# Optimization experiments

Measured on AMD Instinct MI355X. Metric: run time of the kernel, lower is better.

Reference implementation:

```python
import math
import jax, jax.numpy as jnp
import numpy as np

N_HEADS = 16

def setup_inputs() -> dict:
    key = jax.random.key(0)
    k1, k2, k3 = jax.random.split(key, 3)
    B, T, C = 4, 2048, 1024
    alpha = 0.5
    std = alpha * (1.0 / C) ** 0.5
    x = jax.random.normal(k1, (B, T, C), dtype=jnp.float32)
    w_attn = jax.random.normal(k2, (C, 3 * C), dtype=jnp.float32) * std
    b_attn = jnp.zeros((3 * C,), dtype=jnp.float32)
    w_proj = jax.random.normal(k3, (C, C), dtype=jnp.float32) * std
    b_proj = jnp.zeros((C,), dtype=jnp.float32)
    return {"x": x, "w_attn": w_attn, "b_attn": b_attn, "w_proj": w_proj, "b_proj": b_proj}

def reference(x, w_attn, b_attn, w_proj, b_proj):
    B, T, C = x.shape
    H = N_HEADS
    D = C // H
    qkv = x @ w_attn + b_attn                      # [B,T,3C]
    q, k, v = jnp.split(qkv, 3, axis=-1)
    # [B,T,C] -> [B,H,T,D]
    q = q.reshape(B, T, H, D).transpose(0, 2, 1, 3)
    k = k.reshape(B, T, H, D).transpose(0, 2, 1, 3)
    v = v.reshape(B, T, H, D).transpose(0, 2, 1, 3)
    att = jnp.einsum('bhqd,bhkd->bhqk', q, k) * (1.0 / math.sqrt(D))
    causal = jnp.tril(jnp.ones((T, T), dtype=bool))
    att = jnp.where(causal, att, -jnp.inf)
    att = jax.nn.softmax(att, axis=-1)
    y = jnp.einsum('bhqk,bhkd->bhqd', att, v)      # [B,H,T,D]
    y = y.transpose(0, 2, 1, 3).reshape(B, T, C)
    return y @ w_proj + b_proj
```

## Files before the change

kernel.cpp:

```cpp
#include <hip/hip_runtime.h>
#include <hip/hip_bf16.h>

typedef __bf16 bf16x8 __attribute__((ext_vector_type(8)));
typedef float f32x4 __attribute__((ext_vector_type(4)));
typedef unsigned short u16x8 __attribute__((ext_vector_type(8)));
typedef unsigned short u16x4 __attribute__((ext_vector_type(4)));

#define HB 16
#define TT 2048
#define CCH 1024
#define DD 64

#define AS1 __attribute__((address_space(1)))
#define AS3 __attribute__((address_space(3)))
#define GL16(gp, lp) __builtin_amdgcn_global_load_lds((const AS1 void*)(gp), (AS3 void*)(lp), 16, 0, 0)

__device__ __forceinline__ unsigned short f2bf(float f) {
  union { __hip_bfloat16 h; unsigned short u; } cv;
  cv.h = __float2bfloat16(f);
  return cv.u;
}

__device__ __forceinline__ f32x4 mfma16(bf16x8 a, bf16x8 b, f32x4 c) {
  return __builtin_amdgcn_mfma_f32_16x16x32_bf16(a, b, c, 0, 0, 0);
}


__global__ __launch_bounds__(256) void cvt_f32_bf16(const float* __restrict__ in,
                                                    unsigned short* __restrict__ out,
                                                    int n4) {
  int i = blockIdx.x * 256 + threadIdx.x;
  if (i >= n4) return;
  float4 v = reinterpret_cast<const float4*>(in)[i];
  u16x4 o;
  o.x = f2bf(v.x); o.y = f2bf(v.y); o.z = f2bf(v.z); o.w = f2bf(v.w);
  *reinterpret_cast<u16x4*>(out + (size_t)i * 4) = o;
}

__global__ __launch_bounds__(256) void transpose_cvt(const float* __restrict__ w,
                                                     unsigned short* __restrict__ wt,
                                                     int N) {
  __shared__ unsigned short t[32][33];
  int nb = blockIdx.x * 32, kb = blockIdx.y * 32;
  int tx = threadIdx.x & 31, ty = threadIdx.x >> 5;
  #pragma unroll
  for (int r = 0; r < 32; r += 8)
    t[ty + r][tx] = f2bf(w[(size_t)(kb + ty + r) * N + nb + tx]);
  __syncthreads();
  #pragma unroll
  for (int r = 0; r < 32; r += 8)
    wt[(size_t)(nb + ty + r) * 1024 + kb + tx] = t[tx][ty + r];
}


template <int EPI>
__global__ __launch_bounds__(256) void gemm_bf16(
    const unsigned short* __restrict__ A,
    const unsigned short* __restrict__ Bt,
    const float* __restrict__ bias,
    float* __restrict__ outf,
    unsigned short* __restrict__ qb,
    unsigned short* __restrict__ kb,
    unsigned short* __restrict__ vt,
    int nbx, int wpx) {
  __shared__ unsigned short As[8192];
  __shared__ unsigned short Bs[8192];
  const int bid = blockIdx.x;
  const int work = (bid & 7) * wpx + (bid >> 3);
  const int m0 = (work / nbx) * 128, n0 = (work % nbx) * 128;
  const int tid = threadIdx.x;
  const int lane = tid & 63;
  const int wid = tid >> 6;
  const int r16 = lane & 15, g = lane >> 4;
  const int wm = wid >> 1, wn = wid & 1;
  const int srow = tid >> 3;
  const int schx = (tid & 7) ^ (srow & 7);

  f32x4 acc[4][4];
  #pragma unroll
  for (int i = 0; i < 4; ++i)
    #pragma unroll
    for (int j = 0; j < 4; ++j) acc[i][j] = (f32x4){0.f, 0.f, 0.f, 0.f};

  const int rx = r16 & 7;

  for (int kt = 0; kt < 1024; kt += 64) {
    #pragma unroll
    for (int i = 0; i < 4; ++i) {
      const int row = i * 32 + srow;
      GL16(A + (size_t)(m0 + row) * 1024 + kt + schx * 8, As + i * 2048 + tid * 8);
    }
    #pragma unroll
    for (int i = 0; i < 4; ++i) {
      const int row = i * 32 + srow;
      GL16(Bt + (size_t)(n0 + row) * 1024 + kt + schx * 8, Bs + i * 2048 + tid * 8);
    }
    __syncthreads();
    #pragma unroll
    for (int h = 0; h < 2; ++h) {
      bf16x8 af[4], bfr[4];
      #pragma unroll
      for (int i = 0; i < 4; ++i)
        af[i] = *reinterpret_cast<const bf16x8*>(
            &As[(wm * 64 + i * 16 + r16) * 64 + ((g + 4 * h) ^ rx) * 8]);
      #pragma unroll
      for (int j = 0; j < 4; ++j)
        bfr[j] = *reinterpret_cast<const bf16x8*>(
            &Bs[(wn * 64 + j * 16 + r16) * 64 + ((g + 4 * h) ^ rx) * 8]);
      #pragma unroll
      for (int i = 0; i < 4; ++i)
        #pragma unroll
        for (int j = 0; j < 4; ++j)
          acc[i][j] = mfma16(af[i], bfr[j], acc[i][j]);
    }
    __syncthreads();
  }

  #pragma unroll
  for (int i = 0; i < 4; ++i) {
    #pragma unroll
    for (int j = 0; j < 4; ++j) {
      const int n = n0 + wn * 64 + j * 16 + r16;
      const int mbase = m0 + wm * 64 + i * 16 + g * 4;
      const float bi = bias[n];
      if (EPI == 1) {
        #pragma unroll
        for (int r = 0; r < 4; ++r)
          outf[(size_t)(mbase + r) * 1024 + n] = acc[i][j][r] + bi;
      } else {
        const int which = n >> 10;
        const int cc2 = n & 1023;
        const int h = cc2 >> 6, d = cc2 & 63;
        const int b = mbase >> 11, t = mbase & 2047;
        if (which == 2) {
          u16x4 o;
          #pragma unroll
          for (int r = 0; r < 4; ++r) o[r] = f2bf(acc[i][j][r] + bi);
          *reinterpret_cast<u16x4*>(
              &vt[(((size_t)b * HB + h) * DD + d) * TT + t]) = o;
        } else {
          unsigned short* dst = (which == 0) ? qb : kb;
          const float sc = (which == 0) ? 0.18033688011112042f : 1.0f;
          #pragma unroll
          for (int r = 0; r < 4; ++r)
            dst[(((size_t)b * HB + h) * TT + (t + r)) * DD + d] =
                f2bf((acc[i][j][r] + bi) * sc);
        }
      }
    }
  }
}


__global__ __launch_bounds__(512, 2) void attn_kernel(
    const unsigned short* __restrict__ qg_,
    const unsigned short* __restrict__ kg_,
    const unsigned short* __restrict__ vtg_,
    unsigned short* __restrict__ yb) {
  const int bid = blockIdx.x;
  const int work = (bid & 7) * 64 + (bid >> 3);
  const int bh = work >> 3;
  const int jb = work & 7;
  const int tid = threadIdx.x;
  const int wid = tid >> 6;
  const int lane = tid & 63;
  const int r16 = lane & 15, g = lane >> 4;
  const unsigned short* Q = qg_ + (size_t)bh * TT * DD;
  const unsigned short* K = kg_ + (size_t)bh * TT * DD;
  const unsigned short* Vt = vtg_ + (size_t)bh * DD * TT;
  const int b = bh >> 4, h = bh & 15;

  __shared__ unsigned short smem[2][16384];

  const int krow0 = tid >> 3;
  const int kchx = (tid & 7) ^ (krow0 & 7);
  const int vd0 = tid >> 4;
  const int vchx = (tid & 15) ^ (vd0 & 7);
  const int rx = r16 & 7;

#define STAGE(bi, kvb_) do {                                                      \
    unsigned short* sb_ = &smem[bi][0];                                           \
    const unsigned short* gk_ = K + (size_t)(kvb_) * DD;                          \
    GL16(gk_ + (size_t)krow0 * DD + kchx * 8,              sb_ + tid * 8);        \
    GL16(gk_ + (size_t)(64 + krow0) * DD + kchx * 8,       sb_ + 4096 + tid * 8); \
    GL16(Vt + (size_t)vd0 * TT + (kvb_) + vchx * 8,        sb_ + 8192 + tid * 8); \
    GL16(Vt + (size_t)(32 + vd0) * TT + (kvb_) + vchx * 8, sb_ + 12288 + tid * 8);\
  } while (0)

  #pragma unroll
  for (int part = 0; part < 2; ++part) {
    const int qg0 = (part == 0) ? jb * 128 : (15 - jb) * 128;
    const int nt = (part == 0) ? (jb + 1) : (16 - jb);
    const int qw = qg0 + wid * 16;
    const int q = qw + r16;

    bf16x8 qf0 = *reinterpret_cast<const bf16x8*>(&Q[(size_t)q * DD + g * 8]);
    bf16x8 qf1 = *reinterpret_cast<const bf16x8*>(&Q[(size_t)q * DD + 32 + g * 8]);

    f32x4 yacc[4];
    #pragma unroll
    for (int db = 0; db < 4; ++db) yacc[db] = (f32x4){0.f, 0.f, 0.f, 0.f};
    float m = -1e30f, l = 0.f;

    STAGE(0, 0);
    if (nt > 1) {
      STAGE(1, 128);
      asm volatile("s_waitcnt vmcnt(4)" ::: "memory");
    } else {
      asm volatile("s_waitcnt vmcnt(0)" ::: "memory");
    }
    __builtin_amdgcn_s_barrier();

    for (int t = 0; t < nt; ++t) {
      const int kvb = t * 128;
      const unsigned short* sK = &smem[t & 1][0];
      const unsigned short* sV = &smem[t & 1][8192];

      float s[8][4];
      #pragma unroll
      for (int c = 0; c < 8; ++c) {
        bf16x8 kfa = *reinterpret_cast<const bf16x8*>(
            &sK[(c * 16 + r16) * 64 + (g ^ rx) * 8]);
        bf16x8 kfb = *reinterpret_cast<const bf16x8*>(
            &sK[(c * 16 + r16) * 64 + ((g + 4) ^ rx) * 8]);
        f32x4 z = (f32x4){0.f, 0.f, 0.f, 0.f};
        z = mfma16(kfa, qf0, z);
        z = mfma16(kfb, qf1, z);
        #pragma unroll
        for (int r = 0; r < 4; ++r) s[c][r] = z[r];
      }

      float mx = -1e30f;
      if (t == nt - 1) {
        #pragma unroll
        for (int c = 0; c < 8; ++c)
          #pragma unroll
          for (int r = 0; r < 4; ++r) {
            if (kvb + c * 16 + 4 * g + r > q) s[c][r] = -1e30f;
            mx = fmaxf(mx, s[c][r]);
          }
      } else {
        #pragma unroll
        for (int c = 0; c < 8; ++c)
          #pragma unroll
          for (int r = 0; r < 4; ++r) mx = fmaxf(mx, s[c][r]);
      }
      mx = fmaxf(mx, __shfl_xor(mx, 16));
      mx = fmaxf(mx, __shfl_xor(mx, 32));

      if (!__all(mx <= m + 8.f)) {
        const float mn = fmaxf(m, mx);
        const float al = exp2f(m - mn);
        m = mn;
        l *= al;
        #pragma unroll
        for (int db = 0; db < 4; ++db)
          #pragma unroll
          for (int r = 0; r < 4; ++r) yacc[db][r] *= al;
      }
      float rs = 0.f;
      #pragma unroll
      for (int c = 0; c < 8; ++c)
        #pragma unroll
        for (int r = 0; r < 4; ++r) {
          s[c][r] = exp2f(s[c][r] - m);
          rs += s[c][r];
        }
      rs += __shfl_xor(rs, 16);
      rs += __shfl_xor(rs, 32);
      l += rs;

      const int s0l = r16 + 16 * ((2 * g) & 3);
      const int s1l = r16 + 16 * ((2 * g + 1) & 3);
      #pragma unroll
      for (int kk = 0; kk < 4; ++kk) {
        unsigned x0, x1, y0, y1;
        asm("v_cvt_pk_bf16_f32 %0, %1, %2" : "=v"(x0) : "v"(s[2*kk][0]), "v"(s[2*kk][1]));
        asm("v_cvt_pk_bf16_f32 %0, %1, %2" : "=v"(x1) : "v"(s[2*kk][2]), "v"(s[2*kk][3]));
        asm("v_cvt_pk_bf16_f32 %0, %1, %2" : "=v"(y0) : "v"(s[2*kk+1][0]), "v"(s[2*kk+1][1]));
        asm("v_cvt_pk_bf16_f32 %0, %1, %2" : "=v"(y1) : "v"(s[2*kk+1][2]), "v"(s[2*kk+1][3]));
        unsigned a0 = __shfl((int)x0, s0l, 64);
        unsigned b0 = __shfl((int)y0, s0l, 64);
        unsigned a1 = __shfl((int)x1, s0l, 64);
        unsigned b1 = __shfl((int)y1, s0l, 64);
        unsigned a2 = __shfl((int)x0, s1l, 64);
        unsigned b2 = __shfl((int)y0, s1l, 64);
        unsigned a3 = __shfl((int)x1, s1l, 64);
        unsigned b3 = __shfl((int)y1, s1l, 64);
        union { unsigned w[4]; bf16x8 v; } pf;
        pf.w[0] = (g < 2) ? a0 : b0;
        pf.w[1] = (g < 2) ? a1 : b1;
        pf.w[2] = (g < 2) ? a2 : b2;
        pf.w[3] = (g < 2) ? a3 : b3;
        #pragma unroll
        for (int db = 0; db < 4; ++db) {
          bf16x8 vf = *reinterpret_cast<const bf16x8*>(
              &sV[(db * 16 + r16) * 128 + ((kk * 4 + g) ^ rx) * 8]);
          yacc[db] = mfma16(vf, pf.v, yacc[db]);
        }
      }

      __syncthreads();
      if (t + 2 < nt) STAGE(t & 1, (t + 2) * 128);
    }

    const float rl = 1.0f / l;
    #pragma unroll
    for (int db = 0; db < 4; ++db) {
      u16x4 o;
      #pragma unroll
      for (int r = 0; r < 4; ++r) o[r] = f2bf(yacc[db][r] * rl);
      *reinterpret_cast<u16x4*>(
          &yb[((size_t)b * TT + q) * CCH + h * DD + db * 16 + 4 * g]) = o;
    }
  }
#undef STAGE
}


extern "C" void kernel_launch(void* const* d_in, const int* in_sizes, int n_in,
                              void* d_out, int out_size, void* d_ws, size_t ws_size,
                              hipStream_t stream) {
  const float* x      = (const float*)d_in[0];
  const float* w_attn = (const float*)d_in[1];
  const float* b_attn = (const float*)d_in[2];
  const float* w_proj = (const float*)d_in[3];
  const float* b_proj = (const float*)d_in[4];
  float* out = (float*)d_out;
  char* ws = (char*)d_ws;

  unsigned short* xb  = (unsigned short*)(ws + 0);
  unsigned short* wat = (unsigned short*)(ws + 16777216);
  unsigned short* wpt = (unsigned short*)(ws + 23068672);
  unsigned short* qb  = (unsigned short*)(ws + 25165824);
  unsigned short* kb  = (unsigned short*)(ws + 41943040);
  unsigned short* vt  = (unsigned short*)(ws + 58720256);
  unsigned short* yb  = (unsigned short*)(ws + 75497472);

  cvt_f32_bf16<<<(8192 * 1024 / 4 + 255) / 256, 256, 0, stream>>>(x, xb, 8192 * 1024 / 4);
  transpose_cvt<<<dim3(3072 / 32, 32), 256, 0, stream>>>(w_attn, wat, 3072);
  transpose_cvt<<<dim3(1024 / 32, 32), 256, 0, stream>>>(w_proj, wpt, 1024);

  gemm_bf16<0><<<1536, 256, 0, stream>>>(
      xb, wat, b_attn, nullptr, qb, kb, vt, 24, 192);

  attn_kernel<<<512, 512, 0, stream>>>(qb, kb, vt, yb);

  gemm_bf16<1><<<512, 256, 0, stream>>>(
      yb, wpt, b_proj, out, nullptr, nullptr, nullptr, 8, 64);
}
```

Baseline: 186.8 us.

## Software-pipeline QK^T ahead of softmax/PV with split triple-buffered K staging

Restructures the attention loop so the QK^T MFMAs for tile t are issued before the softmax and PV of tile t-1, letting the matrix-core work overlap the exp/reduction VALU work. K and V staging are split into separate LDS buffers (three for K, two for V) so K can be prefetched two tiles ahead and V one tile ahead. It also defers the row-sum cross-lane reduction to the end, reduces the row max only when a rescale is needed, and uses s_setprio around the MFMA blocks. In exchange it holds more registers for the extra score tile and uses more LDS, which may reduce occupancy. The prologue now waits for all initial loads with vmcnt(0).

Result: slower. 203.6 us (+9.0%).

```diff
diff --git a/kernel.cpp b/kernel.cpp
--- a/kernel.cpp
+++ b/kernel.cpp
@@ -170,7 +170,8 @@
   const unsigned short* Vt = vtg_ + (size_t)bh * DD * TT;
   const int b = bh >> 4, h = bh & 15;
 
-  __shared__ unsigned short smem[2][16384];
+  __shared__ unsigned short kbuf[3][8192];
+  __shared__ unsigned short vbuf[2][8192];
 
   const int krow0 = tid >> 3;
   const int kchx = (tid & 7) ^ (krow0 & 7);
@@ -178,13 +179,14 @@
   const int vchx = (tid & 15) ^ (vd0 & 7);
   const int rx = r16 & 7;
 
-#define STAGE(bi, kvb_) do {                                                      \
-    unsigned short* sb_ = &smem[bi][0];                                           \
-    const unsigned short* gk_ = K + (size_t)(kvb_) * DD;                          \
-    GL16(gk_ + (size_t)krow0 * DD + kchx * 8,              sb_ + tid * 8);        \
-    GL16(gk_ + (size_t)(64 + krow0) * DD + kchx * 8,       sb_ + 4096 + tid * 8); \
-    GL16(Vt + (size_t)vd0 * TT + (kvb_) + vchx * 8,        sb_ + 8192 + tid * 8); \
-    GL16(Vt + (size_t)(32 + vd0) * TT + (kvb_) + vchx * 8, sb_ + 12288 + tid * 8);\
+#define SK(bi_, kvb_) do {                                                     \
+    const unsigned short* gk_ = K + (size_t)(kvb_) * DD;                       \
+    GL16(gk_ + (size_t)krow0 * DD + kchx * 8,        &kbuf[bi_][tid * 8]);     \
+    GL16(gk_ + (size_t)(64 + krow0) * DD + kchx * 8, &kbuf[bi_][4096 + tid * 8]); \
+  } while (0)
+#define SV(bi_, kvb_) do {                                                     \
+    GL16(Vt + (size_t)vd0 * TT + (kvb_) + vchx * 8,        &vbuf[bi_][tid * 8]); \
+    GL16(Vt + (size_t)(32 + vd0) * TT + (kvb_) + vchx * 8, &vbuf[bi_][4096 + tid * 8]); \
   } while (0)
 
   #pragma unroll
@@ -200,78 +202,47 @@
     f32x4 yacc[4];
     #pragma unroll
     for (int db = 0; db < 4; ++db) yacc[db] = (f32x4){0.f, 0.f, 0.f, 0.f};
-    float m = -1e30f, l = 0.f;
-
-    STAGE(0, 0);
-    if (nt > 1) {
-      STAGE(1, 128);
-      asm volatile("s_waitcnt vmcnt(4)" ::: "memory");
-    } else {
-      asm volatile("s_waitcnt vmcnt(0)" ::: "memory");
-    }
-    __builtin_amdgcn_s_barrier();
-
-    for (int t = 0; t < nt; ++t) {
-      const int kvb = t * 128;
-      const unsigned short* sK = &smem[t & 1][0];
-      const unsigned short* sV = &smem[t & 1][8192];
-
-      float s[8][4];
-      #pragma unroll
-      for (int c = 0; c < 8; ++c) {
-        bf16x8 kfa = *reinterpret_cast<const bf16x8*>(
-            &sK[(c * 16 + r16) * 64 + (g ^ rx) * 8]);
-        bf16x8 kfb = *reinterpret_cast<const bf16x8*>(
-            &sK[(c * 16 + r16) * 64 + ((g + 4) ^ rx) * 8]);
-        f32x4 z = (f32x4){0.f, 0.f, 0.f, 0.f};
-        z = mfma16(kfa, qf0, z);
-        z = mfma16(kfb, qf1, z);
-        #pragma unroll
-        for (int r = 0; r < 4; ++r) s[c][r] = z[r];
-      }
-
-      float mx = -1e30f;
-      if (t == nt - 1) {
+    float m = -1e30f, lpart = 0.f;
+    float s[8][4];
+
+    const int s0l = r16 + 16 * ((2 * g) & 3);
+    const int s1l = r16 + 16 * ((2 * g + 1) & 3);
+
+    auto softmax_pv = [&](const unsigned short* sV, bool do_mask, int kvb_) {
+      if (do_mask) {
         #pragma unroll
         for (int c = 0; c < 8; ++c)
           #pragma unroll
-          for (int r = 0; r < 4; ++r) {
-            if (kvb + c * 16 + 4 * g + r > q) s[c][r] = -1e30f;
-            mx = fmaxf(mx, s[c][r]);
-          }
-      } else {
-        #pragma unroll
-        for (int c = 0; c < 8; ++c)
-          #pragma unroll
-          for (int r = 0; r < 4; ++r) mx = fmaxf(mx, s[c][r]);
-      }
-      mx = fmaxf(mx, __shfl_xor(mx, 16));
-      mx = fmaxf(mx, __shfl_xor(mx, 32));
-
-      if (!__all(mx <= m + 8.f)) {
-        const float mn = fmaxf(m, mx);
+          for (int r = 0; r < 4; ++r)
+            if (kvb_ + c * 16 + 4 * g + r > q) s[c][r] = -1e30f;
+      }
+      float mc[8];
+      #pragma unroll
+      for (int c = 0; c < 8; ++c)
+        mc[c] = fmaxf(fmaxf(s[c][0], s[c][1]), fmaxf(s[c][2], s[c][3]));
+      float mxl = fmaxf(fmaxf(fmaxf(mc[0], mc[1]), fmaxf(mc[2], mc[3])),
+                        fmaxf(fmaxf(mc[4], mc[5]), fmaxf(mc[6], mc[7])));
+      if (!__all(mxl <= m + 8.f)) {
+        mxl = fmaxf(mxl, __shfl_xor(mxl, 16));
+        mxl = fmaxf(mxl, __shfl_xor(mxl, 32));
+        const float mn = fmaxf(m, mxl);
         const float al = exp2f(m - mn);
         m = mn;
-        l *= al;
+        lpart *= al;
         #pragma unroll
         for (int db = 0; db < 4; ++db)
           #pragma unroll
           for (int r = 0; r < 4; ++r) yacc[db][r] *= al;
       }
-      float rs = 0.f;
-      #pragma unroll
-      for (int c = 0; c < 8; ++c)
-        #pragma unroll
-        for (int r = 0; r < 4; ++r) {
-          s[c][r] = exp2f(s[c][r] - m);
-          rs += s[c][r];
-        }
-      rs += __shfl_xor(rs, 16);
-      rs += __shfl_xor(rs, 32);
-      l += rs;
-
-      const int s0l = r16 + 16 * ((2 * g) & 3);
-      const int s1l = r16 + 16 * ((2 * g + 1) & 3);
+      float sc2[8];
+      #pragma unroll
+      for (int c = 0; c < 8; ++c) {
+        #pragma unroll
+        for (int r = 0; r < 4; ++r) s[c][r] = exp2f(s[c][r] - m);
+        sc2[c] = (s[c][0] + s[c][1]) + (s[c][2] + s[c][3]);
+      }
+      lpart += ((sc2[0] + sc2[1]) + (sc2[2] + sc2[3])) +
+               ((sc2[4] + sc2[5]) + (sc2[6] + sc2[7]));
       #pragma unroll
       for (int kk = 0; kk < 4; ++kk) {
         unsigned x0, x1, y0, y1;
@@ -292,19 +263,64 @@
         pf.w[1] = (g < 2) ? a1 : b1;
         pf.w[2] = (g < 2) ? a2 : b2;
         pf.w[3] = (g < 2) ? a3 : b3;
+        __builtin_amdgcn_s_setprio(1);
         #pragma unroll
         for (int db = 0; db < 4; ++db) {
           bf16x8 vf = *reinterpret_cast<const bf16x8*>(
               &sV[(db * 16 + r16) * 128 + ((kk * 4 + g) ^ rx) * 8]);
           yacc[db] = mfma16(vf, pf.v, yacc[db]);
         }
-      }
+        __builtin_amdgcn_s_setprio(0);
+      }
+    };
+
+    __syncthreads();
+    SK(0, 0);
+    SV(0, 0);
+    if (nt > 1) SK(1, 128);
+    asm volatile("s_waitcnt vmcnt(0)" ::: "memory");
+    __builtin_amdgcn_s_barrier();
+
+    int kc = 0;
+    for (int t = 0; t < nt; ++t) {
+      const unsigned short* sK = &kbuf[kc][0];
+      float sn[8][4];
+      __builtin_amdgcn_s_setprio(1);
+      #pragma unroll
+      for (int c = 0; c < 8; ++c) {
+        bf16x8 kfa = *reinterpret_cast<const bf16x8*>(
+            &sK[(c * 16 + r16) * 64 + (g ^ rx) * 8]);
+        bf16x8 kfb = *reinterpret_cast<const bf16x8*>(
+            &sK[(c * 16 + r16) * 64 + ((g + 4) ^ rx) * 8]);
+        f32x4 z = (f32x4){0.f, 0.f, 0.f, 0.f};
+        z = mfma16(kfa, qf0, z);
+        z = mfma16(kfb, qf1, z);
+        #pragma unroll
+        for (int r = 0; r < 4; ++r) sn[c][r] = z[r];
+      }
+      __builtin_amdgcn_s_setprio(0);
+
+      if (t > 0) softmax_pv(&vbuf[(t - 1) & 1][0], false, 0);
+
+      #pragma unroll
+      for (int c = 0; c < 8; ++c)
+        #pragma unroll
+        for (int r = 0; r < 4; ++r) s[c][r] = sn[c][r];
 
       __syncthreads();
-      if (t + 2 < nt) STAGE(t & 1, (t + 2) * 128);
-    }
-
-    const float rl = 1.0f / l;
+      if (t + 2 < nt) {
+        int k2 = kc + 2; if (k2 >= 3) k2 -= 3;
+        SK(k2, (t + 2) * 128);
+      }
+      if (t + 1 < nt) SV((t + 1) & 1, (t + 1) * 128);
+      kc = (kc == 2) ? 0 : kc + 1;
+    }
+
+    softmax_pv(&vbuf[(nt - 1) & 1][0], true, (nt - 1) * 128);
+
+    lpart += __shfl_xor(lpart, 16);
+    lpart += __shfl_xor(lpart, 32);
+    const float rl = 1.0f / lpart;
     #pragma unroll
     for (int db = 0; db < 4; ++db) {
       u16x4 o;
@@ -314,7 +330,8 @@
           &yb[((size_t)b * TT + q) * CCH + h * DD + db * 16 + 4 * g]) = o;
     }
   }
-#undef STAGE
+#undef SK
+#undef SV
 }
 
 
```

## Rewrite attention with 32x32 MFMA, 32-query waves, 64-key tiles and permlane swap

Applied to the files above, without the earlier changes.

Rebuilds the flash-attention kernel around 32x32x16 bf16 MFMA. Each of 4 waves now owns 32 query rows, keys and values are staged in 64-key tiles, and waves skip key tiles beyond their own causal limit. The P-matrix reshuffle uses v_permlane32_swap instead of many ds shuffles, the row-max reduction across lanes drops to one xor shuffle taken only on rescale, and s_setprio is raised around the MFMA blocks. The aim is to cut shuffle and LDS traffic and wasted causal work, at the cost of fewer threads per block, a smaller LDS tile and more synchronisations per key range.

After: 181.1 us. 3.0% less time.

```diff
diff --git a/kernel.cpp b/kernel.cpp
--- a/kernel.cpp
+++ b/kernel.cpp
@@ -3,6 +3,7 @@
 
 typedef __bf16 bf16x8 __attribute__((ext_vector_type(8)));
 typedef float f32x4 __attribute__((ext_vector_type(4)));
+typedef float f32x16 __attribute__((ext_vector_type(16)));
 typedef unsigned short u16x8 __attribute__((ext_vector_type(8)));
 typedef unsigned short u16x4 __attribute__((ext_vector_type(4)));
 
@@ -21,8 +22,24 @@
   return cv.u;
 }
 
+__device__ __forceinline__ unsigned pack2(float lo, float hi) {
+  unsigned r;
+  asm("v_cvt_pk_bf16_f32 %0, %1, %2" : "=v"(r) : "v"(lo), "v"(hi));
+  return r;
+}
+
 __device__ __forceinline__ f32x4 mfma16(bf16x8 a, bf16x8 b, f32x4 c) {
   return __builtin_amdgcn_mfma_f32_16x16x32_bf16(a, b, c, 0, 0, 0);
+}
+__device__ __forceinline__ f32x16 mfma32(bf16x8 a, bf16x8 b, f32x16 c) {
+  return __builtin_amdgcn_mfma_f32_32x32x16_bf16(a, b, c, 0, 0, 0);
+}
+
+__device__ __forceinline__ f32x16 zero16() {
+  f32x16 z;
+  #pragma unroll
+  for (int r = 0; r < 16; ++r) z[r] = 0.f;
+  return z;
 }
 
 
@@ -152,7 +169,7 @@
 }
 
 
-__global__ __launch_bounds__(512, 2) void attn_kernel(
+__global__ __launch_bounds__(256, 2) void attn_kernel(
     const unsigned short* __restrict__ qg_,
     const unsigned short* __restrict__ kg_,
     const unsigned short* __restrict__ vtg_,
@@ -164,47 +181,52 @@
   const int tid = threadIdx.x;
   const int wid = tid >> 6;
   const int lane = tid & 63;
-  const int r16 = lane & 15, g = lane >> 4;
+  const int l31 = lane & 31, h = lane >> 5;
+  const int lx = lane & 7;
   const unsigned short* Q = qg_ + (size_t)bh * TT * DD;
   const unsigned short* K = kg_ + (size_t)bh * TT * DD;
   const unsigned short* Vt = vtg_ + (size_t)bh * DD * TT;
-  const int b = bh >> 4, h = bh & 15;
-
-  __shared__ unsigned short smem[2][16384];
+  const int b = bh >> 4, hd = bh & 15;
+
+  __shared__ unsigned short kbuf[2][4096];
+  __shared__ unsigned short vbuf[2][4096];
 
   const int krow0 = tid >> 3;
-  const int kchx = (tid & 7) ^ (krow0 & 7);
-  const int vd0 = tid >> 4;
-  const int vchx = (tid & 15) ^ (vd0 & 7);
-  const int rx = r16 & 7;
-
-#define STAGE(bi, kvb_) do {                                                      \
-    unsigned short* sb_ = &smem[bi][0];                                           \
-    const unsigned short* gk_ = K + (size_t)(kvb_) * DD;                          \
-    GL16(gk_ + (size_t)krow0 * DD + kchx * 8,              sb_ + tid * 8);        \
-    GL16(gk_ + (size_t)(64 + krow0) * DD + kchx * 8,       sb_ + 4096 + tid * 8); \
-    GL16(Vt + (size_t)vd0 * TT + (kvb_) + vchx * 8,        sb_ + 8192 + tid * 8); \
-    GL16(Vt + (size_t)(32 + vd0) * TT + (kvb_) + vchx * 8, sb_ + 12288 + tid * 8);\
+  const int chx = (tid & 7) ^ (krow0 & 7);
+
+#define SK(bi_, kvb_) do {                                                   \
+    const unsigned short* gk_ = K + (size_t)((kvb_) + krow0) * DD + chx * 8; \
+    GL16(gk_,            &kbuf[bi_][tid * 8]);                               \
+    GL16(gk_ + 32 * DD,  &kbuf[bi_][2048 + tid * 8]);                        \
+  } while (0)
+#define SV(bi_, kvb_) do {                                                   \
+    const unsigned short* gv_ = Vt + (size_t)krow0 * TT + (kvb_) + chx * 8;  \
+    GL16(gv_,            &vbuf[bi_][tid * 8]);                               \
+    GL16(gv_ + 32 * TT,  &vbuf[bi_][2048 + tid * 8]);                        \
   } while (0)
 
   #pragma unroll
   for (int part = 0; part < 2; ++part) {
     const int qg0 = (part == 0) ? jb * 128 : (15 - jb) * 128;
-    const int nt = (part == 0) ? (jb + 1) : (16 - jb);
-    const int qw = qg0 + wid * 16;
-    const int q = qw + r16;
-
-    bf16x8 qf0 = *reinterpret_cast<const bf16x8*>(&Q[(size_t)q * DD + g * 8]);
-    bf16x8 qf1 = *reinterpret_cast<const bf16x8*>(&Q[(size_t)q * DD + 32 + g * 8]);
-
-    f32x4 yacc[4];
-    #pragma unroll
-    for (int db = 0; db < 4; ++db) yacc[db] = (f32x4){0.f, 0.f, 0.f, 0.f};
-    float m = -1e30f, l = 0.f;
-
-    STAGE(0, 0);
+    const int nt = (part == 0) ? (jb + 1) * 2 : (16 - jb) * 2;
+    const int qw = qg0 + wid * 32;
+    const int q = qw + l31;
+    const int ntw = ((qw + 31) >> 6) + 1;
+
+    bf16x8 qf[4];
+    #pragma unroll
+    for (int c = 0; c < 4; ++c)
+      qf[c] = *reinterpret_cast<const bf16x8*>(&Q[(size_t)q * DD + c * 16 + h * 8]);
+
+    f32x16 y0 = zero16(), y1 = zero16();
+    float m = -1e30f, lp = 0.f;
+
+    __syncthreads();
+    SK(0, 0);
+    SV(0, 0);
     if (nt > 1) {
-      STAGE(1, 128);
+      SK(1, 64);
+      SV(1, 64);
       asm volatile("s_waitcnt vmcnt(4)" ::: "memory");
     } else {
       asm volatile("s_waitcnt vmcnt(0)" ::: "memory");
@@ -212,109 +234,127 @@
     __builtin_amdgcn_s_barrier();
 
     for (int t = 0; t < nt; ++t) {
-      const int kvb = t * 128;
-      const unsigned short* sK = &smem[t & 1][0];
-      const unsigned short* sV = &smem[t & 1][8192];
-
-      float s[8][4];
-      #pragma unroll
-      for (int c = 0; c < 8; ++c) {
-        bf16x8 kfa = *reinterpret_cast<const bf16x8*>(
-            &sK[(c * 16 + r16) * 64 + (g ^ rx) * 8]);
-        bf16x8 kfb = *reinterpret_cast<const bf16x8*>(
-            &sK[(c * 16 + r16) * 64 + ((g + 4) ^ rx) * 8]);
-        f32x4 z = (f32x4){0.f, 0.f, 0.f, 0.f};
-        z = mfma16(kfa, qf0, z);
-        z = mfma16(kfb, qf1, z);
-        #pragma unroll
-        for (int r = 0; r < 4; ++r) s[c][r] = z[r];
+      const unsigned short* sK = kbuf[t & 1];
+      const unsigned short* sV = vbuf[t & 1];
+
+      if (t < ntw) {
+        const int kvb = t * 64;
+
+        f32x16 z0 = zero16(), z1 = zero16();
+        __builtin_amdgcn_s_setprio(1);
+        #pragma unroll
+        for (int c = 0; c < 4; ++c) {
+          bf16x8 kf = *reinterpret_cast<const bf16x8*>(
+              &sK[l31 * 64 + (((2 * c + h) ^ lx)) * 8]);
+          z0 = mfma32(kf, qf[c], z0);
+        }
+        #pragma unroll
+        for (int c = 0; c < 4; ++c) {
+          bf16x8 kf = *reinterpret_cast<const bf16x8*>(
+              &sK[(32 + l31) * 64 + (((2 * c + h) ^ lx)) * 8]);
+          z1 = mfma32(kf, qf[c], z1);
+        }
+        __builtin_amdgcn_s_setprio(0);
+
+        if (t == ntw - 1) {
+          #pragma unroll
+          for (int r = 0; r < 16; ++r) {
+            const int kv0 = kvb + (r & 3) + 8 * (r >> 2) + 4 * h;
+            if (kv0 > q) z0[r] = -1e30f;
+            if (kv0 + 32 > q) z1[r] = -1e30f;
+          }
+        }
+
+        float mq[8];
+        #pragma unroll
+        for (int i = 0; i < 4; ++i) {
+          mq[i] = fmaxf(fmaxf(z0[4 * i], z0[4 * i + 1]),
+                        fmaxf(z0[4 * i + 2], z0[4 * i + 3]));
+          mq[4 + i] = fmaxf(fmaxf(z1[4 * i], z1[4 * i + 1]),
+                            fmaxf(z1[4 * i + 2], z1[4 * i + 3]));
+        }
+        float mx = fmaxf(fmaxf(fmaxf(mq[0], mq[1]), fmaxf(mq[2], mq[3])),
+                         fmaxf(fmaxf(mq[4], mq[5]), fmaxf(mq[6], mq[7])));
+
+        if (!__all(mx <= m + 8.f)) {
+          mx = fmaxf(mx, __shfl_xor(mx, 32));
+          const float mn = fmaxf(m, mx);
+          const float al = exp2f(m - mn);
+          m = mn;
+          lp *= al;
+          #pragma unroll
+          for (int r = 0; r < 16; ++r) { y0[r] *= al; y1[r] *= al; }
+        }
+
+        float sq[8];
+        #pragma unroll
+        for (int i = 0; i < 4; ++i) {
+          #pragma unroll
+          for (int r = 0; r < 4; ++r) {
+            z0[4 * i + r] = exp2f(z0[4 * i + r] - m);
+            z1[4 * i + r] = exp2f(z1[4 * i + r] - m);
+          }
+          sq[i] = (z0[4 * i] + z0[4 * i + 1]) + (z0[4 * i + 2] + z0[4 * i + 3]);
+          sq[4 + i] = (z1[4 * i] + z1[4 * i + 1]) + (z1[4 * i + 2] + z1[4 * i + 3]);
+        }
+        lp += ((sq[0] + sq[1]) + (sq[2] + sq[3])) +
+              ((sq[4] + sq[5]) + (sq[6] + sq[7]));
+
+        unsigned pw[16];
+        #pragma unroll
+        for (int w = 0; w < 8; ++w) {
+          pw[w] = pack2(z0[2 * w], z0[2 * w + 1]);
+          pw[8 + w] = pack2(z1[2 * w], z1[2 * w + 1]);
+        }
+        #pragma unroll
+        for (int kb = 0; kb < 4; ++kb) {
+          asm("v_permlane32_swap_b32 %0, %1"
+              : "+v"(pw[4 * kb]), "+v"(pw[4 * kb + 2]));
+          asm("v_permlane32_swap_b32 %0, %1"
+              : "+v"(pw[4 * kb + 1]), "+v"(pw[4 * kb + 3]));
+        }
+
+        __builtin_amdgcn_s_setprio(1);
+        #pragma unroll
+        for (int kb = 0; kb < 4; ++kb) {
+          union { unsigned w[4]; bf16x8 v; } pf;
+          pf.w[0] = pw[4 * kb];
+          pf.w[1] = pw[4 * kb + 1];
+          pf.w[2] = pw[4 * kb + 2];
+          pf.w[3] = pw[4 * kb + 3];
+          bf16x8 vf0 = *reinterpret_cast<const bf16x8*>(
+              &sV[l31 * 64 + (((2 * kb + h) ^ lx)) * 8]);
+          y0 = mfma32(vf0, pf.v, y0);
+          bf16x8 vf1 = *reinterpret_cast<const bf16x8*>(
+              &sV[(32 + l31) * 64 + (((2 * kb + h) ^ lx)) * 8]);
+          y1 = mfma32(vf1, pf.v, y1);
+        }
+        __builtin_amdgcn_s_setprio(0);
       }
 
-      float mx = -1e30f;
-      if (t == nt - 1) {
-        #pragma unroll
-        for (int c = 0; c < 8; ++c)
-          #pragma unroll
-          for (int r = 0; r < 4; ++r) {
-            if (kvb + c * 16 + 4 * g + r > q) s[c][r] = -1e30f;
-            mx = fmaxf(mx, s[c][r]);
-          }
-      } else {
-        #pragma unroll
-        for (int c = 0; c < 8; ++c)
-          #pragma unroll
-          for (int r = 0; r < 4; ++r) mx = fmaxf(mx, s[c][r]);
+      __syncthreads();
+      if (t + 2 < nt) {
+        SK(t & 1, (t + 2) * 64);
+        SV(t & 1, (t + 2) * 64);
       }
-      mx = fmaxf(mx, __shfl_xor(mx, 16));
-      mx = fmaxf(mx, __shfl_xor(mx, 32));
-
-      if (!__all(mx <= m + 8.f)) {
-        const float mn = fmaxf(m, mx);
-        const float al = exp2f(m - mn);
-        m = mn;
-        l *= al;
-        #pragma unroll
-        for (int db = 0; db < 4; ++db)
-          #pragma unroll
-          for (int r = 0; r < 4; ++r) yacc[db][r] *= al;
-      }
-      float rs = 0.f;
-      #pragma unroll
-      for (int c = 0; c < 8; ++c)
-        #pragma unroll
-        for (int r = 0; r < 4; ++r) {
-          s[c][r] = exp2f(s[c][r] - m);
-          rs += s[c][r];
-        }
-      rs += __shfl_xor(rs, 16);
-      rs += __shfl_xor(rs, 32);
-      l += rs;
-
-      const int s0l = r16 + 16 * ((2 * g) & 3);
-      const int s1l = r16 + 16 * ((2 * g + 1) & 3);
-      #pragma unroll
-      for (int kk = 0; kk < 4; ++kk) {
-        unsigned x0, x1, y0, y1;
-        asm("v_cvt_pk_bf16_f32 %0, %1, %2" : "=v"(x0) : "v"(s[2*kk][0]), "v"(s[2*kk][1]));
-        asm("v_cvt_pk_bf16_f32 %0, %1, %2" : "=v"(x1) : "v"(s[2*kk][2]), "v"(s[2*kk][3]));
-        asm("v_cvt_pk_bf16_f32 %0, %1, %2" : "=v"(y0) : "v"(s[2*kk+1][0]), "v"(s[2*kk+1][1]));
-        asm("v_cvt_pk_bf16_f32 %0, %1, %2" : "=v"(y1) : "v"(s[2*kk+1][2]), "v"(s[2*kk+1][3]));
-        unsigned a0 = __shfl((int)x0, s0l, 64);
-        unsigned b0 = __shfl((int)y0, s0l, 64);
-        unsigned a1 = __shfl((int)x1, s0l, 64);
-        unsigned b1 = __shfl((int)y1, s0l, 64);
-        unsigned a2 = __shfl((int)x0, s1l, 64);
-        unsigned b2 = __shfl((int)y0, s1l, 64);
-        unsigned a3 = __shfl((int)x1, s1l, 64);
-        unsigned b3 = __shfl((int)y1, s1l, 64);
-        union { unsigned w[4]; bf16x8 v; } pf;
-        pf.w[0] = (g < 2) ? a0 : b0;
-        pf.w[1] = (g < 2) ? a1 : b1;
-        pf.w[2] = (g < 2) ? a2 : b2;
-        pf.w[3] = (g < 2) ? a3 : b3;
-        #pragma unroll
-        for (int db = 0; db < 4; ++db) {
-          bf16x8 vf = *reinterpret_cast<const bf16x8*>(
-              &sV[(db * 16 + r16) * 128 + ((kk * 4 + g) ^ rx) * 8]);
-          yacc[db] = mfma16(vf, pf.v, yacc[db]);
-        }
-      }
-
-      __syncthreads();
-      if (t + 2 < nt) STAGE(t & 1, (t + 2) * 128);
-    }
-
-    const float rl = 1.0f / l;
-    #pragma unroll
-    for (int db = 0; db < 4; ++db) {
-      u16x4 o;
-      #pragma unroll
-      for (int r = 0; r < 4; ++r) o[r] = f2bf(yacc[db][r] * rl);
-      *reinterpret_cast<u16x4*>(
-          &yb[((size_t)b * TT + q) * CCH + h * DD + db * 16 + 4 * g]) = o;
+    }
+
+    lp += __shfl_xor(lp, 32);
+    const float rl = 1.0f / lp;
+    const size_t obase = ((size_t)b * TT + q) * CCH + hd * DD;
+    #pragma unroll
+    for (int g4 = 0; g4 < 4; ++g4) {
+      const int d0 = 8 * g4 + 4 * h;
+      unsigned w0 = pack2(y0[4 * g4] * rl, y0[4 * g4 + 1] * rl);
+      unsigned w1 = pack2(y0[4 * g4 + 2] * rl, y0[4 * g4 + 3] * rl);
+      *reinterpret_cast<uint2*>(&yb[obase + d0]) = make_uint2(w0, w1);
+      unsigned w2 = pack2(y1[4 * g4] * rl, y1[4 * g4 + 1] * rl);
+      unsigned w3 = pack2(y1[4 * g4 + 2] * rl, y1[4 * g4 + 3] * rl);
+      *reinterpret_cast<uint2*>(&yb[obase + 32 + d0]) = make_uint2(w2, w3);
     }
   }
-#undef STAGE
+#undef SK
+#undef SV
 }
 
 
@@ -344,7 +384,7 @@
   gemm_bf16<0><<<1536, 256, 0, stream>>>(
       xb, wat, b_attn, nullptr, qb, kb, vt, 24, 192);
 
-  attn_kernel<<<512, 512, 0, stream>>>(qb, kb, vt, yb);
+  attn_kernel<<<512, 256, 0, stream>>>(qb, kb, vt, yb);
 
   gemm_bf16<1><<<512, 256, 0, stream>>>(
       yb, wpt, b_proj, out, nullptr, nullptr, nullptr, 8, 64);
```
